# Performance work log

Hardware: AMD Instinct MI355X
Metric: run time of the kernel (lower is better)

Reference implementation:

```python
import jax, jax.numpy as jnp
import numpy as np

N_NODES = 50000
N_EDGES = 500000
IN_FEATS = 64
HIDDEN = 64
OUT_FEATS = 8
N_LAYERS = 6
NEG_SLOPE = 0.2
LN_EPS = 1e-5


def setup_inputs() -> dict:
    key = jax.random.key(0)
    ks = jax.random.split(key, 12)
    s_in = 1.0 / np.sqrt(IN_FEATS)
    s_h = 1.0 / np.sqrt(HIDDEN)
    return {
        "nodes": jax.random.normal(ks[0], (N_NODES, IN_FEATS), jnp.float32),
        "src": jax.random.randint(ks[1], (N_EDGES,), 0, N_NODES, jnp.int32),
        "dst": jax.random.randint(ks[2], (N_EDGES,), 0, N_NODES, jnp.int32),
        "w_in": jax.random.normal(ks[3], (IN_FEATS, HIDDEN), jnp.float32) * s_in,
        "b_in": jnp.zeros((HIDDEN,), jnp.float32),
        "w_src": jax.random.normal(ks[4], (N_LAYERS, HIDDEN, HIDDEN), jnp.float32) * s_h,
        "b_src": jnp.zeros((N_LAYERS, HIDDEN), jnp.float32),
        "w_dst": jax.random.normal(ks[5], (N_LAYERS, HIDDEN, HIDDEN), jnp.float32) * s_h,
        "b_dst": jnp.zeros((N_LAYERS, HIDDEN), jnp.float32),
        "attn": jax.random.normal(ks[6], (N_LAYERS, HIDDEN), jnp.float32) * s_h,
        "gamma": jnp.ones((N_LAYERS, HIDDEN), jnp.float32),
        "beta": jnp.zeros((N_LAYERS, HIDDEN), jnp.float32),
        "w_out": jax.random.normal(ks[7], (HIDDEN, OUT_FEATS), jnp.float32) * s_h,
        "b_out": jnp.zeros((OUT_FEATS,), jnp.float32),
    }


def _layernorm(x, g, b):
    m = jnp.mean(x, axis=-1, keepdims=True)
    v = jnp.mean(jnp.square(x - m), axis=-1, keepdims=True)
    return (x - m) * jax.lax.rsqrt(v + LN_EPS) * g + b


def _gatv2(h, src, dst, ws, bs, wd, bd, a, n_nodes):
    # GATv2Conv, num_heads=1 (DGL semantics)
    fs = h @ ws + bs                                  # [N, H] fc_src
    fd = h @ wd + bd                                  # [N, H] fc_dst
    e = jax.nn.leaky_relu(fs[src] + fd[dst], NEG_SLOPE)  # [E, H]
    score = e @ a                                     # [E]
    # segment softmax over incoming edges of each dst node
    mx = jax.ops.segment_max(score, dst, num_segments=n_nodes)
    ex = jnp.exp(score - mx[dst])
    denom = jax.ops.segment_sum(ex, dst, num_segments=n_nodes)
    alpha = ex / denom[dst]                           # [E]
    return jax.ops.segment_sum(alpha[:, None] * fs[src], dst, num_segments=n_nodes)


def reference(nodes, src, dst, w_in, b_in, w_src, b_src, w_dst, b_dst, attn, gamma, beta, w_out, b_out):
    n = nodes.shape[0]
    h = nodes @ w_in + b_in
    for i in range(N_LAYERS):
        t = _gatv2(h, src, dst, w_src[i], b_src[i], w_dst[i], b_dst[i], attn[i], n)
        t = _layernorm(t, gamma[i], beta[i])
        h = h + jax.nn.gelu(t, approximate=False)
    return h @ w_out + b_out
```

## Files before the change

kernel.cpp:

```cpp
#include <hip/hip_runtime.h>
#include <math.h>

#define N_NODES 50000
#define N_EDGES 500000
#define NLAYERS 6
#define NEG_SLOPE 0.2f
#define LN_EPS 1e-5f
#define SCAN_B 1024
#define NSCAN_BLOCKS ((N_NODES + SCAN_B - 1) / SCAN_B)
#define LOG2E 1.4426950408889634f

typedef __attribute__((ext_vector_type(8))) short short8;
typedef __attribute__((ext_vector_type(4))) float f32x4;

__device__ __forceinline__ float wave_sum64(float v) {
#pragma unroll
    for (int m = 32; m >= 1; m >>= 1) v += __shfl_xor(v, m, 64);
    return v;
}

__device__ __forceinline__ int wave_incl_scan(int v, int lane) {
#pragma unroll
    for (int offs = 1; offs < 64; offs <<= 1) {
        int t = __shfl_up(v, offs, 64);
        if (lane >= offs) v += t;
    }
    return v;
}

__device__ __forceinline__ unsigned bf16_rne(float v) {
    unsigned u = __float_as_uint(v);
    return (u + 0x7fffu + ((u >> 16) & 1u)) >> 16;
}

__device__ __forceinline__ float fast_exp2(float x) {
    float r;
    asm("v_exp_f32 %0, %1" : "=v"(r) : "v"(x));
    return r;
}

__global__ void count_deg(const int* __restrict__ dst, int* __restrict__ deg) {
    int i = blockIdx.x * blockDim.x + threadIdx.x;
    if (i < N_EDGES) atomicAdd(&deg[dst[i]], 1);
}

__global__ void scan1(const int* __restrict__ deg, int* __restrict__ row_ptr,
                      int* __restrict__ bsum) {
    int i = blockIdx.x * SCAN_B + threadIdx.x;
    int lane = threadIdx.x & 63, wv = threadIdx.x >> 6;
    int v = (i < N_NODES) ? deg[i] : 0;
    int incl = wave_incl_scan(v, lane);
    __shared__ int wtot[16];
    if (lane == 63) wtot[wv] = incl;
    __syncthreads();
    if (wv == 0) {
        int wval = (lane < 16) ? wtot[lane] : 0;
        int ws = wave_incl_scan(wval, lane);
        if (lane < 16) wtot[lane] = ws - wval;
    }
    __syncthreads();
    int excl = incl - v + wtot[wv];
    if (i < N_NODES) row_ptr[i] = excl;
    if (threadIdx.x == SCAN_B - 1) bsum[blockIdx.x] = excl + v;
}

__global__ void scan2(const int* __restrict__ bsum, int* __restrict__ boffs) {
    int lane = threadIdx.x;
    int v = (lane < NSCAN_BLOCKS) ? bsum[lane] : 0;
    int incl = wave_incl_scan(v, lane);
    if (lane < NSCAN_BLOCKS) boffs[lane] = incl - v;
}

__global__ void scan3(int* __restrict__ row_ptr, const int* __restrict__ boffs,
                      int* __restrict__ pos) {
    int i = blockIdx.x * SCAN_B + threadIdx.x;
    if (i < N_NODES) {
        int r = row_ptr[i] + boffs[blockIdx.x];
        row_ptr[i] = r;
        pos[i] = r;
    }
    if (i == 0) row_ptr[N_NODES] = N_EDGES;
}

__global__ void scatter_edges(const int* __restrict__ dst, const int* __restrict__ src,
                              int* __restrict__ pos, int* __restrict__ srcs) {
    int i = blockIdx.x * blockDim.x + threadIdx.x;
    if (i < N_EDGES) {
        int p = atomicAdd(&pos[dst[i]], 1);
        srcs[p] = src[i];
    }
}

__global__ void pack_w(const float* __restrict__ w_in, const float* __restrict__ w_src,
                       const float* __restrict__ w_dst, unsigned short* __restrict__ wpk_hi,
                       unsigned short* __restrict__ wpk_lo) {
    int b = blockIdx.x;
    const float* W = (b == 0) ? w_in
                              : (b <= 6 ? w_src + (size_t)(b - 1) * 4096
                                        : w_dst + (size_t)(b - 7) * 4096);
    unsigned short* hi = wpk_hi + (size_t)b * 4096;
    unsigned short* lo = wpk_lo + (size_t)b * 4096;
    for (int idx = threadIdx.x; idx < 4096; idx += 256) {
        int t = idx >> 10;
        int s = (idx >> 9) & 1;
        int l = (idx >> 3) & 63;
        int j = idx & 7;
        int row = s * 32 + (l >> 4) * 8 + j;
        int col = t * 16 + (l & 15);
        float v = W[row * 64 + col];
        unsigned rh = bf16_rne(v);
        float hf = __uint_as_float(rh << 16);
        unsigned rl = bf16_rne(v - hf);
        hi[idx] = (unsigned short)rh;
        lo[idx] = (unsigned short)rl;
    }
}

__device__ __forceinline__ void load_split8(const float* __restrict__ p, short8& hi, short8& lo) {
    float4 x0 = *(const float4*)p;
    float4 x1 = *(const float4*)(p + 4);
    float v[8] = {x0.x, x0.y, x0.z, x0.w, x1.x, x1.y, x1.z, x1.w};
#pragma unroll
    for (int j = 0; j < 8; ++j) {
        unsigned rh = bf16_rne(v[j]);
        float hf = __uint_as_float(rh << 16);
        unsigned rl = bf16_rne(v[j] - hf);
        hi[j] = (short)rh;
        lo[j] = (short)rl;
    }
}

__device__ __forceinline__ void mfma_16rows(const short8 ah0, const short8 ah1, const short8 al0,
                                            const short8 al1,
                                            const unsigned short* __restrict__ whi,
                                            const unsigned short* __restrict__ wlo, int lane,
                                            f32x4 acc[4]) {
#pragma unroll
    for (int t = 0; t < 4; ++t) {
#pragma unroll
        for (int s = 0; s < 2; ++s) {
            const size_t boff = ((size_t)((t * 2 + s) * 64 + lane)) * 8;
            short8 bh = *(const short8*)(whi + boff);
            short8 bl = *(const short8*)(wlo + boff);
            short8 a_h = s ? ah1 : ah0;
            short8 a_l = s ? al1 : al0;
            acc[t] = __builtin_amdgcn_mfma_f32_16x16x32_bf16(a_h, bh, acc[t], 0, 0, 0);
            acc[t] = __builtin_amdgcn_mfma_f32_16x16x32_bf16(a_l, bh, acc[t], 0, 0, 0);
            acc[t] = __builtin_amdgcn_mfma_f32_16x16x32_bf16(a_h, bl, acc[t], 0, 0, 0);
        }
    }
}

__global__ void mfma_in_proj(const float* __restrict__ X, const unsigned short* __restrict__ whi,
                             const unsigned short* __restrict__ wlo,
                             const float* __restrict__ bias, float* __restrict__ H) {
    int lane = threadIdx.x & 63, wv = threadIdx.x >> 6;
    int R = blockIdx.x * 64 + wv * 16;
    int arow = min(R + (lane & 15), N_NODES - 1);
    const float* p = X + (size_t)arow * 64 + (lane >> 4) * 8;
    short8 ah0, ah1, al0, al1;
    load_split8(p, ah0, al0);
    load_split8(p + 32, ah1, al1);
    f32x4 acc[4];
    f32x4 z = {0.f, 0.f, 0.f, 0.f};
#pragma unroll
    for (int t = 0; t < 4; ++t) acc[t] = z;
    mfma_16rows(ah0, ah1, al0, al1, whi, wlo, lane, acc);
    int crow = R + (lane >> 4) * 4;
#pragma unroll
    for (int t = 0; t < 4; ++t) {
        int col = t * 16 + (lane & 15);
        float bv = bias[col];
#pragma unroll
        for (int r = 0; r < 4; ++r) {
            int row = crow + r;
            if (row < N_NODES) H[(size_t)row * 64 + col] = acc[t][r] + bv;
        }
    }
}

__global__ void mfma_dual(const float* __restrict__ X, const unsigned short* __restrict__ wshi,
                          const unsigned short* __restrict__ wslo, const float* __restrict__ bs,
                          const unsigned short* __restrict__ wdhi,
                          const unsigned short* __restrict__ wdlo, const float* __restrict__ bd,
                          float* __restrict__ FS, float* __restrict__ FD) {
    int lane = threadIdx.x & 63, wv = threadIdx.x >> 6;
    int R = blockIdx.x * 64 + wv * 16;
    int arow = min(R + (lane & 15), N_NODES - 1);
    const float* p = X + (size_t)arow * 64 + (lane >> 4) * 8;
    short8 ah0, ah1, al0, al1;
    load_split8(p, ah0, al0);
    load_split8(p + 32, ah1, al1);
    f32x4 accS[4], accD[4];
    f32x4 z = {0.f, 0.f, 0.f, 0.f};
#pragma unroll
    for (int t = 0; t < 4; ++t) {
        accS[t] = z;
        accD[t] = z;
    }
    mfma_16rows(ah0, ah1, al0, al1, wshi, wslo, lane, accS);
    mfma_16rows(ah0, ah1, al0, al1, wdhi, wdlo, lane, accD);
    int crow = R + (lane >> 4) * 4;
#pragma unroll
    for (int t = 0; t < 4; ++t) {
        int col = t * 16 + (lane & 15);
        float bsv = bs[col], bdv = bd[col];
#pragma unroll
        for (int r = 0; r < 4; ++r) {
            int row = crow + r;
            if (row < N_NODES) {
                FS[(size_t)row * 64 + col] = accS[t][r] + bsv;
                FD[(size_t)row * 64 + col] = accD[t][r] + bdv;
            }
        }
    }
}

#define WPB 4
__global__ void node_fused_kernel(const float* __restrict__ fs, const float* __restrict__ fd,
                                  const int* __restrict__ row_ptr, const int* __restrict__ srcs,
                                  const float* __restrict__ attn, const float* __restrict__ gamma,
                                  const float* __restrict__ beta, float* __restrict__ h) {
    __shared__ float xpose[WPB][64];
    int lane = threadIdx.x & 63;
    int wv = threadIdx.x >> 6;
    int q = lane >> 4;
    int ql = lane & 15;
    int f0 = ql << 2;
    int n = blockIdx.x * WPB + wv;
    if (n >= N_NODES) return;
    float gL = gamma[lane], bL = beta[lane];
    float hval = h[(size_t)n * 64 + lane];
    float4 a4 = *(const float4*)&attn[f0];
    a4.x *= LOG2E;
    a4.y *= LOG2E;
    a4.z *= LOG2E;
    a4.w *= LOG2E;
    int beg = row_ptr[n], end = row_ptr[n + 1];
    int deg = end - beg;
    float4 fd4 = *(const float4*)&fd[(size_t)n * 64 + f0];
    float m = -INFINITY, d = 0.f;
    float4 acc = make_float4(0.f, 0.f, 0.f, 0.f);
    for (int c0 = 0; c0 < deg; c0 += 64) {
        int cl = min(64, deg - c0);
        int sv = (lane < cl) ? srcs[beg + c0 + lane] : 0;
        int nt = (cl + 3) >> 2;
        float4 rowA = make_float4(0.f, 0.f, 0.f, 0.f), rowB = rowA;
        int sid0 = __shfl(sv, q, 64);
        if (q < cl) rowA = *(const float4*)&fs[(size_t)sid0 * 64 + f0];
        int sid1 = __shfl(sv, (4 + q) & 63, 64);
        if (4 + q < cl) rowB = *(const float4*)&fs[(size_t)sid1 * 64 + f0];
        for (int t = 0; t < nt; ++t) {
            int eoff = 4 * t + q;
            bool valid = eoff < cl;
            float4 cur = rowA;
            rowA = rowB;
            int e2 = 4 * (t + 2) + q;
            int sid2 = __shfl(sv, e2 & 63, 64);
            if (e2 < cl) rowB = *(const float4*)&fs[(size_t)sid2 * 64 + f0];
            float vx = cur.x + fd4.x, vy = cur.y + fd4.y;
            float vz = cur.z + fd4.z, vw = cur.w + fd4.w;
            vx = fmaxf(vx, NEG_SLOPE * vx);
            vy = fmaxf(vy, NEG_SLOPE * vy);
            vz = fmaxf(vz, NEG_SLOPE * vz);
            vw = fmaxf(vw, NEG_SLOPE * vw);
            float sp = fmaf(a4.x, vx, fmaf(a4.y, vy, fmaf(a4.z, vz, a4.w * vw)));
            sp += __shfl_xor(sp, 1, 64);
            sp += __shfl_xor(sp, 2, 64);
            sp += __shfl_xor(sp, 4, 64);
            sp += __shfl_xor(sp, 8, 64);
            if (valid) {
                float diff = sp - m;
                if (diff > 8.f) {
                    float sc = fast_exp2(-diff);
                    d *= sc;
                    acc.x *= sc;
                    acc.y *= sc;
                    acc.z *= sc;
                    acc.w *= sc;
                    m = sp;
                    diff = 0.f;
                }
                float w = fast_exp2(diff);
                d += w;
                acc.x = fmaf(w, cur.x, acc.x);
                acc.y = fmaf(w, cur.y, acc.y);
                acc.z = fmaf(w, cur.z, acc.z);
                acc.w = fmaf(w, cur.w, acc.w);
            }
        }
    }
    float mo = fmaxf(m, __shfl_xor(m, 16, 64));
    mo = fmaxf(mo, __shfl_xor(mo, 32, 64));
    float scale = (m == -INFINITY) ? 0.f : fast_exp2(m - mo);
    d *= scale;
    d += __shfl_xor(d, 16, 64);
    d += __shfl_xor(d, 32, 64);
    acc.x *= scale;
    acc.y *= scale;
    acc.z *= scale;
    acc.w *= scale;
    acc.x += __shfl_xor(acc.x, 16, 64);
    acc.y += __shfl_xor(acc.y, 16, 64);
    acc.z += __shfl_xor(acc.z, 16, 64);
    acc.w += __shfl_xor(acc.w, 16, 64);
    acc.x += __shfl_xor(acc.x, 32, 64);
    acc.y += __shfl_xor(acc.y, 32, 64);
    acc.z += __shfl_xor(acc.z, 32, 64);
    acc.w += __shfl_xor(acc.w, 32, 64);
    float inv = (d > 0.f) ? 1.f / d : 0.f;
    acc.x *= inv;
    acc.y *= inv;
    acc.z *= inv;
    acc.w *= inv;
    if (q == 0) *(float4*)&xpose[wv][f0] = acc;
    float val = xpose[wv][lane];
    float mean = wave_sum64(val) * 0.015625f;
    float dev = val - mean;
    float var = wave_sum64(dev * dev) * 0.015625f;
    float rstd = rsqrtf(var + LN_EPS);
    float tval = fmaf(dev * rstd, gL, bL);
    float g = 0.5f * tval * (1.f + erff(tval * 0.70710678118654752f));
    h[(size_t)n * 64 + lane] = hval + g;
}

__global__ void out_proj_kernel(const float* __restrict__ h, const float* __restrict__ W,
                                const float* __restrict__ b, float* __restrict__ out) {
    __shared__ float Ws[64 * 8];
    __shared__ float bs[8];
    __shared__ float Hs[32][65];
    int t = threadIdx.x;
    for (int i = t; i < 512; i += 256) Ws[i] = W[i];
    if (t < 8) bs[t] = b[t];
    int n0 = blockIdx.x * 32;
    for (int i = t; i < 32 * 64; i += 256) {
        int r = i >> 6, c = i & 63;
        int n = n0 + r;
        Hs[r][c] = (n < N_NODES) ? h[(size_t)n * 64 + c] : 0.f;
    }
    __syncthreads();
    int nl = t >> 3, o = t & 7;
    int n = n0 + nl;
    if (n >= N_NODES) return;
    float acc = bs[o];
#pragma unroll
    for (int k = 0; k < 64; ++k) acc = fmaf(Hs[nl][k], Ws[k * 8 + o], acc);
    out[(size_t)n * 8 + o] = acc;
}

extern "C" void kernel_launch(void* const* d_in, const int* in_sizes, int n_in,
                              void* d_out, int out_size, void* d_ws, size_t ws_size,
                              hipStream_t stream) {
    const float* nodes = (const float*)d_in[0];
    const int* src = (const int*)d_in[1];
    const int* dst = (const int*)d_in[2];
    const float* w_in = (const float*)d_in[3];
    const float* b_in = (const float*)d_in[4];
    const float* w_src = (const float*)d_in[5];
    const float* b_src = (const float*)d_in[6];
    const float* w_dst = (const float*)d_in[7];
    const float* b_dst = (const float*)d_in[8];
    const float* attn = (const float*)d_in[9];
    const float* gamma = (const float*)d_in[10];
    const float* beta = (const float*)d_in[11];
    const float* w_out = (const float*)d_in[12];
    const float* b_out = (const float*)d_in[13];
    float* out = (float*)d_out;

    char* ws = (char*)d_ws;
    size_t off = 0;
    auto alloc = [&](size_t bytes) {
        void* p = ws + off;
        off += (bytes + 255) & ~(size_t)255;
        return p;
    };
    float* h = (float*)alloc((size_t)N_NODES * 64 * 4);
    float* fs = (float*)alloc((size_t)N_NODES * 64 * 4);
    float* fd = (float*)alloc((size_t)N_NODES * 64 * 4);
    unsigned short* wpk_hi = (unsigned short*)alloc((size_t)13 * 4096 * 2);
    unsigned short* wpk_lo = (unsigned short*)alloc((size_t)13 * 4096 * 2);
    int* deg = (int*)alloc((size_t)N_NODES * 4);
    int* row_ptr = (int*)alloc((size_t)(N_NODES + 1) * 4);
    int* pos = (int*)alloc((size_t)N_NODES * 4);
    int* srcs = (int*)alloc((size_t)N_EDGES * 4);
    int* bsum = (int*)alloc((size_t)NSCAN_BLOCKS * 4);
    int* boffs = (int*)alloc((size_t)NSCAN_BLOCKS * 4);

    hipMemsetAsync(deg, 0, (size_t)N_NODES * 4, stream);
    count_deg<<<(N_EDGES + 255) / 256, 256, 0, stream>>>(dst, deg);
    scan1<<<NSCAN_BLOCKS, SCAN_B, 0, stream>>>(deg, row_ptr, bsum);
    scan2<<<1, 64, 0, stream>>>(bsum, boffs);
    scan3<<<NSCAN_BLOCKS, SCAN_B, 0, stream>>>(row_ptr, boffs, pos);
    scatter_edges<<<(N_EDGES + 255) / 256, 256, 0, stream>>>(dst, src, pos, srcs);

    pack_w<<<13, 256, 0, stream>>>(w_in, w_src, w_dst, wpk_hi, wpk_lo);

    mfma_in_proj<<<(N_NODES + 63) / 64, 256, 0, stream>>>(nodes, wpk_hi, wpk_lo, b_in, h);

    for (int l = 0; l < NLAYERS; ++l) {
        mfma_dual<<<(N_NODES + 63) / 64, 256, 0, stream>>>(
            h, wpk_hi + (size_t)(1 + l) * 4096, wpk_lo + (size_t)(1 + l) * 4096,
            b_src + (size_t)l * 64, wpk_hi + (size_t)(7 + l) * 4096,
            wpk_lo + (size_t)(7 + l) * 4096, b_dst + (size_t)l * 64, fs, fd);
        node_fused_kernel<<<(N_NODES + WPB - 1) / WPB, 256, 0, stream>>>(
            fs, fd, row_ptr, srcs, attn + (size_t)l * 64, gamma + (size_t)l * 64,
            beta + (size_t)l * 64, h);
    }

    out_proj_kernel<<<(N_NODES + 31) / 32, 256, 0, stream>>>(h, w_out, b_out, out);
}
```

Before: 358.3 us.

## Unroll edge loop to two independent online-softmax streams and fold scan2 into scan3

The per-node aggregation loop now handles 8 edges per iteration in two independent online-softmax accumulators, which are merged at the end. Loads are made unconditional by clamping edge indices, and invalid lanes are masked with a large negative score and a zero weight. The aim is more memory-level parallelism and shorter dependency chains in the gather-bound layer kernel, at the cost of more registers and some wasted loads for low-degree nodes. Separately, the scan2 launch is removed: each scan3 block sums the preceding block totals itself, saving one kernel launch.

```diff
diff --git a/kernel.cpp b/kernel.cpp
--- a/kernel.cpp
+++ b/kernel.cpp
@@ -9,6 +9,7 @@
 #define SCAN_B 1024
 #define NSCAN_BLOCKS ((N_NODES + SCAN_B - 1) / SCAN_B)
 #define LOG2E 1.4426950408889634f
+#define NEG_BIG -3.0e38f
 
 typedef __attribute__((ext_vector_type(8))) short short8;
 typedef __attribute__((ext_vector_type(4))) float f32x4;
@@ -64,18 +65,21 @@
     if (threadIdx.x == SCAN_B - 1) bsum[blockIdx.x] = excl + v;
 }
 
-__global__ void scan2(const int* __restrict__ bsum, int* __restrict__ boffs) {
-    int lane = threadIdx.x;
-    int v = (lane < NSCAN_BLOCKS) ? bsum[lane] : 0;
-    int incl = wave_incl_scan(v, lane);
-    if (lane < NSCAN_BLOCKS) boffs[lane] = incl - v;
-}
-
-__global__ void scan3(int* __restrict__ row_ptr, const int* __restrict__ boffs,
+__global__ void scan3(int* __restrict__ row_ptr, const int* __restrict__ bsum,
                       int* __restrict__ pos) {
-    int i = blockIdx.x * SCAN_B + threadIdx.x;
+    __shared__ int boff_s;
+    int t = threadIdx.x;
+    if (t < 64) {
+        int v = (t < NSCAN_BLOCKS && t < (int)blockIdx.x) ? bsum[t] : 0;
+        v = wave_sum64(__int_as_float(0)) == 0.f ? v : v;
+#pragma unroll
+        for (int m = 32; m >= 1; m >>= 1) v += __shfl_xor(v, m, 64);
+        if (t == 0) boff_s = v;
+    }
+    __syncthreads();
+    int i = blockIdx.x * SCAN_B + t;
     if (i < N_NODES) {
-        int r = row_ptr[i] + boffs[blockIdx.x];
+        int r = row_ptr[i] + boff_s;
         row_ptr[i] = r;
         pos[i] = r;
     }
@@ -239,60 +243,100 @@
     int beg = row_ptr[n], end = row_ptr[n + 1];
     int deg = end - beg;
     float4 fd4 = *(const float4*)&fd[(size_t)n * 64 + f0];
-    float m = -INFINITY, d = 0.f;
-    float4 acc = make_float4(0.f, 0.f, 0.f, 0.f);
+    float m0 = NEG_BIG, d0 = 0.f;
+    float m1 = NEG_BIG, d1 = 0.f;
+    float4 acc0 = make_float4(0.f, 0.f, 0.f, 0.f), acc1 = acc0;
     for (int c0 = 0; c0 < deg; c0 += 64) {
         int cl = min(64, deg - c0);
+        int clm1 = cl - 1;
         int sv = (lane < cl) ? srcs[beg + c0 + lane] : 0;
-        int nt = (cl + 3) >> 2;
-        float4 rowA = make_float4(0.f, 0.f, 0.f, 0.f), rowB = rowA;
-        int sid0 = __shfl(sv, q, 64);
-        if (q < cl) rowA = *(const float4*)&fs[(size_t)sid0 * 64 + f0];
-        int sid1 = __shfl(sv, (4 + q) & 63, 64);
-        if (4 + q < cl) rowB = *(const float4*)&fs[(size_t)sid1 * 64 + f0];
-        for (int t = 0; t < nt; ++t) {
-            int eoff = 4 * t + q;
-            bool valid = eoff < cl;
-            float4 cur = rowA;
-            rowA = rowB;
-            int e2 = 4 * (t + 2) + q;
-            int sid2 = __shfl(sv, e2 & 63, 64);
-            if (e2 < cl) rowB = *(const float4*)&fs[(size_t)sid2 * 64 + f0];
-            float vx = cur.x + fd4.x, vy = cur.y + fd4.y;
-            float vz = cur.z + fd4.z, vw = cur.w + fd4.w;
-            vx = fmaxf(vx, NEG_SLOPE * vx);
-            vy = fmaxf(vy, NEG_SLOPE * vy);
-            vz = fmaxf(vz, NEG_SLOPE * vz);
-            vw = fmaxf(vw, NEG_SLOPE * vw);
-            float sp = fmaf(a4.x, vx, fmaf(a4.y, vy, fmaf(a4.z, vz, a4.w * vw)));
-            sp += __shfl_xor(sp, 1, 64);
-            sp += __shfl_xor(sp, 2, 64);
-            sp += __shfl_xor(sp, 4, 64);
-            sp += __shfl_xor(sp, 8, 64);
-            if (valid) {
-                float diff = sp - m;
-                if (diff > 8.f) {
-                    float sc = fast_exp2(-diff);
-                    d *= sc;
-                    acc.x *= sc;
-                    acc.y *= sc;
-                    acc.z *= sc;
-                    acc.w *= sc;
-                    m = sp;
-                    diff = 0.f;
-                }
-                float w = fast_exp2(diff);
-                d += w;
-                acc.x = fmaf(w, cur.x, acc.x);
-                acc.y = fmaf(w, cur.y, acc.y);
-                acc.z = fmaf(w, cur.z, acc.z);
-                acc.w = fmaf(w, cur.w, acc.w);
+        int nu = (cl + 7) >> 3;
+        int sidA = __shfl(sv, min(q, clm1), 64);
+        int sidB = __shfl(sv, min(4 + q, clm1), 64);
+        float4 rA = *(const float4*)&fs[(size_t)sidA * 64 + f0];
+        float4 rB = *(const float4*)&fs[(size_t)sidB * 64 + f0];
+        for (int u = 0; u < nu; ++u) {
+            int eA = 8 * u + q;
+            int eB = eA + 4;
+            int sidA2 = __shfl(sv, min(eA + 8, clm1), 64);
+            int sidB2 = __shfl(sv, min(eB + 8, clm1), 64);
+            float4 cA = rA, cB = rB;
+            rA = *(const float4*)&fs[(size_t)sidA2 * 64 + f0];
+            rB = *(const float4*)&fs[(size_t)sidB2 * 64 + f0];
+            float vax = cA.x + fd4.x, vay = cA.y + fd4.y;
+            float vaz = cA.z + fd4.z, vaw = cA.w + fd4.w;
+            float vbx = cB.x + fd4.x, vby = cB.y + fd4.y;
+            float vbz = cB.z + fd4.z, vbw = cB.w + fd4.w;
+            vax = fmaxf(vax, NEG_SLOPE * vax);
+            vay = fmaxf(vay, NEG_SLOPE * vay);
+            vaz = fmaxf(vaz, NEG_SLOPE * vaz);
+            vaw = fmaxf(vaw, NEG_SLOPE * vaw);
+            vbx = fmaxf(vbx, NEG_SLOPE * vbx);
+            vby = fmaxf(vby, NEG_SLOPE * vby);
+            vbz = fmaxf(vbz, NEG_SLOPE * vbz);
+            vbw = fmaxf(vbw, NEG_SLOPE * vbw);
+            float spA = fmaf(a4.x, vax, fmaf(a4.y, vay, fmaf(a4.z, vaz, a4.w * vaw)));
+            float spB = fmaf(a4.x, vbx, fmaf(a4.y, vby, fmaf(a4.z, vbz, a4.w * vbw)));
+            spA += __shfl_xor(spA, 1, 64);
+            spB += __shfl_xor(spB, 1, 64);
+            spA += __shfl_xor(spA, 2, 64);
+            spB += __shfl_xor(spB, 2, 64);
+            spA += __shfl_xor(spA, 4, 64);
+            spB += __shfl_xor(spB, 4, 64);
+            spA += __shfl_xor(spA, 8, 64);
+            spB += __shfl_xor(spB, 8, 64);
+            bool vA = eA < cl, vB = eB < cl;
+            spA = vA ? spA : NEG_BIG;
+            spB = vB ? spB : NEG_BIG;
+            float dfA = spA - m0;
+            if (dfA > 8.f) {
+                float sc = fast_exp2(-dfA);
+                d0 *= sc;
+                acc0.x *= sc;
+                acc0.y *= sc;
+                acc0.z *= sc;
+                acc0.w *= sc;
+                m0 = spA;
+                dfA = 0.f;
             }
+            float wA = fast_exp2(dfA);
+            wA = vA ? wA : 0.f;
+            d0 += wA;
+            acc0.x = fmaf(wA, cA.x, acc0.x);
+            acc0.y = fmaf(wA, cA.y, acc0.y);
+            acc0.z = fmaf(wA, cA.z, acc0.z);
+            acc0.w = fmaf(wA, cA.w, acc0.w);
+            float dfB = spB - m1;
+            if (dfB > 8.f) {
+                float sc = fast_exp2(-dfB);
+                d1 *= sc;
+                acc1.x *= sc;
+                acc1.y *= sc;
+                acc1.z *= sc;
+                acc1.w *= sc;
+                m1 = spB;
+                dfB = 0.f;
+            }
+            float wB = fast_exp2(dfB);
+            wB = vB ? wB : 0.f;
+            d1 += wB;
+            acc1.x = fmaf(wB, cB.x, acc1.x);
+            acc1.y = fmaf(wB, cB.y, acc1.y);
+            acc1.z = fmaf(wB, cB.z, acc1.z);
+            acc1.w = fmaf(wB, cB.w, acc1.w);
         }
     }
+    float m = fmaxf(m0, m1);
+    float s0 = fast_exp2(m0 - m), s1 = fast_exp2(m1 - m);
+    float d = d0 * s0 + d1 * s1;
+    float4 acc;
+    acc.x = acc0.x * s0 + acc1.x * s1;
+    acc.y = acc0.y * s0 + acc1.y * s1;
+    acc.z = acc0.z * s0 + acc1.z * s1;
+    acc.w = acc0.w * s0 + acc1.w * s1;
     float mo = fmaxf(m, __shfl_xor(m, 16, 64));
     mo = fmaxf(mo, __shfl_xor(mo, 32, 64));
-    float scale = (m == -INFINITY) ? 0.f : fast_exp2(m - mo);
+    float scale = fast_exp2(m - mo);
     d *= scale;
     d += __shfl_xor(d, 16, 64);
     d += __shfl_xor(d, 32, 64);
@@ -384,13 +428,11 @@
     int* pos = (int*)alloc((size_t)N_NODES * 4);
     int* srcs = (int*)alloc((size_t)N_EDGES * 4);
     int* bsum = (int*)alloc((size_t)NSCAN_BLOCKS * 4);
-    int* boffs = (int*)alloc((size_t)NSCAN_BLOCKS * 4);
 
     hipMemsetAsync(deg, 0, (size_t)N_NODES * 4, stream);
     count_deg<<<(N_EDGES + 255) / 256, 256, 0, stream>>>(dst, deg);
     scan1<<<NSCAN_BLOCKS, SCAN_B, 0, stream>>>(deg, row_ptr, bsum);
-    scan2<<<1, 64, 0, stream>>>(bsum, boffs);
-    scan3<<<NSCAN_BLOCKS, SCAN_B, 0, stream>>>(row_ptr, boffs, pos);
+    scan3<<<NSCAN_BLOCKS, SCAN_B, 0, stream>>>(row_ptr, bsum, pos);
     scatter_edges<<<(N_EDGES + 255) / 256, 256, 0, stream>>>(dst, src, pos, srcs);
 
     pack_w<<<13, 256, 0, stream>>>(w_in, w_src, w_dst, wpk_hi, wpk_lo);
```

Result: slower. 379.6 us (+6.0%).

## Process nodes in degree-binned order and fold scan2 into scan3

Applied to the files above, without the earlier changes.

Builds a 64-bin degree histogram and a node permutation sorted by in-degree. The fused per-node attention kernel then processes nodes in that order, so waves in one block have similar edge counts and wait less on a long-degree sibling. The separate scan2 launch is removed by having each scan3 block reduce the preceding block sums itself. The cost is indirect node indexing, which makes h/fd accesses less coalesced and scatters writes, plus extra atomics during setup.

```diff
diff --git a/kernel.cpp b/kernel.cpp
--- a/kernel.cpp
+++ b/kernel.cpp
@@ -39,16 +39,19 @@
     return r;
 }
 
-__global__ void count_deg(const int* __restrict__ dst, int* __restrict__ deg) {
+__global__ void count_deg(const int* __restrict__ dst, int* __restrict__ deg,
+                          int* __restrict__ hist) {
+    if (blockIdx.x == 0 && threadIdx.x < 64) hist[threadIdx.x] = 0;
     int i = blockIdx.x * blockDim.x + threadIdx.x;
     if (i < N_EDGES) atomicAdd(&deg[dst[i]], 1);
 }
 
 __global__ void scan1(const int* __restrict__ deg, int* __restrict__ row_ptr,
-                      int* __restrict__ bsum) {
+                      int* __restrict__ bsum, int* __restrict__ hist) {
     int i = blockIdx.x * SCAN_B + threadIdx.x;
     int lane = threadIdx.x & 63, wv = threadIdx.x >> 6;
     int v = (i < N_NODES) ? deg[i] : 0;
+    if (i < N_NODES) atomicAdd(&hist[min(v, 63)], 1);
     int incl = wave_incl_scan(v, lane);
     __shared__ int wtot[16];
     if (lane == 63) wtot[wv] = incl;
@@ -64,18 +67,27 @@
     if (threadIdx.x == SCAN_B - 1) bsum[blockIdx.x] = excl + v;
 }
 
-__global__ void scan2(const int* __restrict__ bsum, int* __restrict__ boffs) {
-    int lane = threadIdx.x;
-    int v = (lane < NSCAN_BLOCKS) ? bsum[lane] : 0;
-    int incl = wave_incl_scan(v, lane);
-    if (lane < NSCAN_BLOCKS) boffs[lane] = incl - v;
-}
-
-__global__ void scan3(int* __restrict__ row_ptr, const int* __restrict__ boffs,
-                      int* __restrict__ pos) {
-    int i = blockIdx.x * SCAN_B + threadIdx.x;
+__global__ void scan3(int* __restrict__ row_ptr, const int* __restrict__ bsum,
+                      int* __restrict__ pos, const int* __restrict__ hist,
+                      int* __restrict__ binpos) {
+    __shared__ int boff_s;
+    int t = threadIdx.x;
+    if (t < 64) {
+        int v = (t < NSCAN_BLOCKS && t < (int)blockIdx.x) ? bsum[t] : 0;
+#pragma unroll
+        for (int m = 32; m >= 1; m >>= 1) v += __shfl_xor(v, m, 64);
+        if (t == 0) boff_s = v;
+    }
+    if (blockIdx.x == 0 && t >= 64 && t < 128) {
+        int lane = t - 64;
+        int v = hist[lane];
+        int incl = wave_incl_scan(v, lane);
+        binpos[lane] = incl - v;
+    }
+    __syncthreads();
+    int i = blockIdx.x * SCAN_B + t;
     if (i < N_NODES) {
-        int r = row_ptr[i] + boffs[blockIdx.x];
+        int r = row_ptr[i] + boff_s;
         row_ptr[i] = r;
         pos[i] = r;
     }
@@ -83,11 +95,18 @@
 }
 
 __global__ void scatter_edges(const int* __restrict__ dst, const int* __restrict__ src,
-                              int* __restrict__ pos, int* __restrict__ srcs) {
+                              int* __restrict__ pos, int* __restrict__ srcs,
+                              const int* __restrict__ deg, int* __restrict__ binpos,
+                              int* __restrict__ perm) {
     int i = blockIdx.x * blockDim.x + threadIdx.x;
     if (i < N_EDGES) {
         int p = atomicAdd(&pos[dst[i]], 1);
         srcs[p] = src[i];
+    }
+    if (i < N_NODES) {
+        int b = min(deg[i], 63);
+        int p = atomicAdd(&binpos[b], 1);
+        perm[p] = i;
     }
 }
 
@@ -219,16 +238,18 @@
 #define WPB 4
 __global__ void node_fused_kernel(const float* __restrict__ fs, const float* __restrict__ fd,
                                   const int* __restrict__ row_ptr, const int* __restrict__ srcs,
-                                  const float* __restrict__ attn, const float* __restrict__ gamma,
-                                  const float* __restrict__ beta, float* __restrict__ h) {
+                                  const int* __restrict__ perm, const float* __restrict__ attn,
+                                  const float* __restrict__ gamma, const float* __restrict__ beta,
+                                  float* __restrict__ h) {
     __shared__ float xpose[WPB][64];
     int lane = threadIdx.x & 63;
     int wv = threadIdx.x >> 6;
     int q = lane >> 4;
     int ql = lane & 15;
     int f0 = ql << 2;
-    int n = blockIdx.x * WPB + wv;
-    if (n >= N_NODES) return;
+    int idx = blockIdx.x * WPB + wv;
+    if (idx >= N_NODES) return;
+    int n = perm[idx];
     float gL = gamma[lane], bL = beta[lane];
     float hval = h[(size_t)n * 64 + lane];
     float4 a4 = *(const float4*)&attn[f0];
@@ -384,14 +405,16 @@
     int* pos = (int*)alloc((size_t)N_NODES * 4);
     int* srcs = (int*)alloc((size_t)N_EDGES * 4);
     int* bsum = (int*)alloc((size_t)NSCAN_BLOCKS * 4);
-    int* boffs = (int*)alloc((size_t)NSCAN_BLOCKS * 4);
+    int* hist = (int*)alloc((size_t)64 * 4);
+    int* binpos = (int*)alloc((size_t)64 * 4);
+    int* perm = (int*)alloc((size_t)N_NODES * 4);
 
     hipMemsetAsync(deg, 0, (size_t)N_NODES * 4, stream);
-    count_deg<<<(N_EDGES + 255) / 256, 256, 0, stream>>>(dst, deg);
-    scan1<<<NSCAN_BLOCKS, SCAN_B, 0, stream>>>(deg, row_ptr, bsum);
-    scan2<<<1, 64, 0, stream>>>(bsum, boffs);
-    scan3<<<NSCAN_BLOCKS, SCAN_B, 0, stream>>>(row_ptr, boffs, pos);
-    scatter_edges<<<(N_EDGES + 255) / 256, 256, 0, stream>>>(dst, src, pos, srcs);
+    count_deg<<<(N_EDGES + 255) / 256, 256, 0, stream>>>(dst, deg, hist);
+    scan1<<<NSCAN_BLOCKS, SCAN_B, 0, stream>>>(deg, row_ptr, bsum, hist);
+    scan3<<<NSCAN_BLOCKS, SCAN_B, 0, stream>>>(row_ptr, bsum, pos, hist, binpos);
+    scatter_edges<<<(N_EDGES + 255) / 256, 256, 0, stream>>>(dst, src, pos, srcs, deg, binpos,
+                                                             perm);
 
     pack_w<<<13, 256, 0, stream>>>(w_in, w_src, w_dst, wpk_hi, wpk_lo);
 
@@ -403,7 +426,7 @@
             b_src + (size_t)l * 64, wpk_hi + (size_t)(7 + l) * 4096,
             wpk_lo + (size_t)(7 + l) * 4096, b_dst + (size_t)l * 64, fs, fd);
         node_fused_kernel<<<(N_NODES + WPB - 1) / WPB, 256, 0, stream>>>(
-            fs, fd, row_ptr, srcs, attn + (size_t)l * 64, gamma + (size_t)l * 64,
+            fs, fd, row_ptr, srcs, perm, attn + (size_t)l * 64, gamma + (size_t)l * 64,
             beta + (size_t)l * 64, h);
     }
 
```

After: 684.3 us. 91.0% more time.
